# Optimization experiments

Measured on AMD Instinct MI355X. Metric: run time of the kernel, lower is better.

## Reference

```python
import jax, jax.numpy as jnp
import numpy as np

B, N, D = 16, 1024, 5
R_HID = 8  # radial MLP hidden width


def setup_inputs() -> dict:
    key = jax.random.key(0)
    ks = jax.random.split(key, 16)
    feats = jax.random.normal(ks[0], (B, N, D), jnp.float32)
    coors = 3.0 * jax.random.normal(ks[1], (B, N, 3), jnp.float32)
    a = jax.random.bernoulli(ks[2], 0.01, (B, N, N))
    adj_mat = a | jnp.swapaxes(a, 1, 2)
    s = 1.0 / np.sqrt(D)
    Wq = s * jax.random.normal(ks[3], (D, D), jnp.float32)
    Wk = s * jax.random.normal(ks[4], (D, D), jnp.float32)
    Wv = s * jax.random.normal(ks[5], (D, D), jnp.float32)
    Wo = s * jax.random.normal(ks[6], (D, D), jnp.float32)
    w_r1 = 0.5 * jax.random.normal(ks[7], (1, R_HID), jnp.float32)
    b_r1 = jnp.zeros((R_HID,), jnp.float32)
    w_r2 = 0.5 * jax.random.normal(ks[8], (R_HID, 1), jnp.float32)
    b_r2 = jnp.zeros((1,), jnp.float32)
    w1 = (1.0 / np.sqrt(D)) * jax.random.normal(ks[9], (D, 128), jnp.float32)
    b1 = jnp.zeros((128,), jnp.float32)
    w2 = (1.0 / np.sqrt(128.0)) * jax.random.normal(ks[10], (128, 3), jnp.float32)
    b2 = jnp.zeros((3,), jnp.float32)
    return dict(feats=feats, coors=coors, adj_mat=adj_mat, Wq=Wq, Wk=Wk, Wv=Wv,
                Wo=Wo, w_r1=w_r1, b_r1=b_r1, w_r2=w_r2, b_r2=b_r2,
                w1=w1, b1=b1, w2=w2, b2=b2)


def _se3_layer(feats, coors, neigh, Wq, Wk, Wv, Wo, w_r1, b_r1, w_r2, b_r2):
    # SE(3)-invariant sparse graph attention on degree-0 channels.
    # Attention logits = content term + radial (distance-only) bias, so the
    # scalar output is invariant to global rotations/translations of coors.
    q = jnp.einsum('bnd,de->bne', feats, Wq)
    k = jnp.einsum('bnd,de->bne', feats, Wk)
    v = jnp.einsum('bnd,de->bne', feats, Wv)
    rel = coors[:, :, None, :] - coors[:, None, :, :]        # [B,N,N,3]
    dist = jnp.sqrt(jnp.sum(rel * rel, axis=-1) + 1e-8)      # [B,N,N]
    h = jax.nn.relu(dist[..., None] * w_r1[0] + b_r1)        # [B,N,N,R_HID]
    rbias = (h @ w_r2)[..., 0] + b_r2[0]                     # [B,N,N]
    scores = jnp.einsum('bid,bjd->bij', q, k) / np.sqrt(q.shape[-1]) + rbias
    scores = jnp.where(neigh, scores, -1e9)
    attn = jax.nn.softmax(scores, axis=-1)
    agg = jnp.einsum('bij,bjd->bid', attn, v)
    return feats + jnp.einsum('bid,de->bie', agg, Wo)        # residual


def reference(feats, coors, adj_mat, Wq, Wk, Wv, Wo, w_r1, b_r1, w_r2, b_r2,
              w1, b1, w2, b2):
    a = adj_mat.astype(jnp.float32)
    # num_adj_degrees=2: attend over 1-hop and 2-hop neighbors (+ self)
    adj2 = jnp.einsum('bij,bjk->bik', a, a) > 0
    eye = jnp.eye(adj_mat.shape[1], dtype=bool)[None]
    neigh = adj_mat | adj2 | eye
    x = _se3_layer(feats, coors, neigh, Wq, Wk, Wv, Wo, w_r1, b_r1, w_r2, b_r2)
    pooled = jnp.mean(x, axis=1)                              # [B, D]
    hdn = jax.nn.relu(pooled @ w1 + b1)
    return hdn @ w2 + b2                                      # [B, 3]
```

## Files before the change

### kernel.cpp

```cpp
#include <hip/hip_runtime.h>
#include <hip/hip_bf16.h>

#define BB 16
#define NN 1024
#define DD 5
#define RH 8

typedef unsigned long long u64;
typedef unsigned int u32;
typedef __hip_bfloat16 bf16;

static __device__ __forceinline__ float tof(bf16 x) { return __bfloat162float(x); }
static __device__ __forceinline__ float ldf(const void* p, long long i, bool f) {
  return f ? ((const float*)p)[i] : tof(((const bf16*)p)[i]);
}

#define LOG2E 1.4426950408889634f
#define PACK_BLOCKS (BB * NN * 16 / 256)
#define KV_BLOCKS (BB * NN / 256)


__global__ __launch_bounds__(256) void k_pack(
    const void* __restrict__ adj, const void* __restrict__ feats,
    const void* __restrict__ coors,
    const void* __restrict__ Wk, const void* __restrict__ Wv,
    const void* __restrict__ Wo,
    u64* __restrict__ adjbits, float4* __restrict__ kvg,
    float* __restrict__ czg, int* __restrict__ gflags,
    float* __restrict__ pooled, int* __restrict__ cntr) {
  __shared__ int sNon01, sNonpair, sLow3;
  __shared__ int sCnt[4];
  __shared__ float wkL[25], wvL[25], woL[25];
  int tid = threadIdx.x;

  if (blockIdx.x >= PACK_BLOCKS) {
    int kb = blockIdx.x - PACK_BLOCKS;
    if (kb == 0) {
      if (tid < BB * DD) pooled[tid] = 0.0f;
      else if (tid < BB * DD + BB) cntr[tid - BB * DD] = 0;
    }
    {
      u32 x = ((const u32*)feats)[tid];
      u32 lo = x & 0xFFFFu;
      int e = (int)((lo >> 7) & 0xFFu);
      bool insane = !(lo == 0u || (e >= 90 && e <= 150));
      u64 m = __ballot(insane);
      if ((tid & 63) == 0) sCnt[tid >> 6] = (int)__popcll(m);
    }
    __syncthreads();
    bool f32 = (sCnt[0] + sCnt[1] + sCnt[2] + sCnt[3]) > 64;
    if (tid < 25) {
      wkL[tid] = ldf(Wk, tid, f32);
      wvL[tid] = ldf(Wv, tid, f32);
      woL[tid] = ldf(Wo, tid, f32);
    }
    if (kb == 0 && tid == 0) gflags[0] = f32 ? 1 : 0;
    __syncthreads();
    long long node = (long long)kb * 256 + tid;
    float f0 = ldf(feats, node * DD + 0, f32), f1 = ldf(feats, node * DD + 1, f32),
          f2 = ldf(feats, node * DD + 2, f32), f3 = ldf(feats, node * DD + 3, f32),
          f4 = ldf(feats, node * DD + 4, f32);
    float k[DD], tv[DD], v[DD];
    #pragma unroll
    for (int e = 0; e < DD; ++e) {
      k[e] = f0 * wkL[e] + f1 * wkL[5 + e] + f2 * wkL[10 + e] + f3 * wkL[15 + e] +
             f4 * wkL[20 + e];
      tv[e] = f0 * wvL[e] + f1 * wvL[5 + e] + f2 * wvL[10 + e] + f3 * wvL[15 + e] +
              f4 * wvL[20 + e];
    }
    #pragma unroll
    for (int e = 0; e < DD; ++e)
      v[e] = tv[0] * woL[e] + tv[1] * woL[5 + e] + tv[2] * woL[10 + e] +
             tv[3] * woL[15 + e] + tv[4] * woL[20 + e];
    float cx = ldf(coors, node * 3 + 0, f32);
    float cy = ldf(coors, node * 3 + 1, f32);
    float cz = ldf(coors, node * 3 + 2, f32);
    kvg[node * 3 + 0] = make_float4(k[0], k[1], k[2], k[3]);
    kvg[node * 3 + 1] = make_float4(k[4], v[0], v[1], v[2]);
    kvg[node * 3 + 2] = make_float4(v[3], v[4], cx, cy);
    czg[node] = cz;
    return;
  }

  if (tid == 0) { sNon01 = 0; sNonpair = 0; sLow3 = 0; }
  __syncthreads();
  {
    const u32* aw = (const u32*)adj;
    int non01 = 0, nonpair = 0, low3 = 0;
    for (int i = tid; i < 4096; i += 256) {
      u32 x = aw[i];
      u32 lo = x & 0xFFFFu, hi = x >> 16;
      non01 |= (x > 1u);
      nonpair |= !((lo == 0u || lo == 0x3F80u) && (hi == 0u || hi == 0x3F80u));
      low3 |= (lo == 0x3F80u);
    }
    if (non01) atomicOr(&sNon01, 1);
    if (nonpair) atomicOr(&sNonpair, 1);
    if (low3) atomicOr(&sLow3, 1);
  }
  __syncthreads();
  int mode;
  if (!sNon01) mode = 0;
  else if (!sNonpair) mode = sLow3 ? 2 : 3;
  else mode = 1;

  int gid = blockIdx.x * 256 + tid;
  int w = gid & 15;
  long long row = gid >> 4;
  long long base = row * NN + (long long)w * 64;
  u64 bits = 0;
  if (mode == 3) {
    const uint4* p = (const uint4*)((const float*)adj + base);
    #pragma unroll
    for (int t = 0; t < 16; ++t) {
      uint4 x = p[t];
      if (x.x << 1) bits |= 1ull << (4 * t + 0);
      if (x.y << 1) bits |= 1ull << (4 * t + 1);
      if (x.z << 1) bits |= 1ull << (4 * t + 2);
      if (x.w << 1) bits |= 1ull << (4 * t + 3);
    }
  } else if (mode == 0) {
    const uint4* p = (const uint4*)((const u32*)adj + base);
    #pragma unroll
    for (int t = 0; t < 16; ++t) {
      uint4 x = p[t];
      if (x.x) bits |= 1ull << (4 * t + 0);
      if (x.y) bits |= 1ull << (4 * t + 1);
      if (x.z) bits |= 1ull << (4 * t + 2);
      if (x.w) bits |= 1ull << (4 * t + 3);
    }
  } else if (mode == 2) {
    const uint4* p = (const uint4*)((const unsigned short*)adj + base);
    #pragma unroll
    for (int t = 0; t < 8; ++t) {
      uint4 x = p[t];
      u32 c[4] = {x.x, x.y, x.z, x.w};
      #pragma unroll
      for (int q = 0; q < 4; ++q) {
        if ((c[q] & 0x7FFFu)) bits |= 1ull << (8 * t + 2 * q + 0);
        if ((c[q] >> 16) & 0x7FFFu) bits |= 1ull << (8 * t + 2 * q + 1);
      }
    }
  } else {
    const uint4* p = (const uint4*)((const unsigned char*)adj + base);
    #pragma unroll
    for (int t = 0; t < 4; ++t) {
      uint4 x = p[t];
      u32 c[4] = {x.x, x.y, x.z, x.w};
      #pragma unroll
      for (int q = 0; q < 4; ++q)
        #pragma unroll
        for (int bb = 0; bb < 4; ++bb)
          if ((c[q] >> (8 * bb)) & 0xFFu) bits |= 1ull << (16 * t + 4 * q + bb);
    }
  }
  adjbits[gid] = bits;
}

__global__ __launch_bounds__(512) void k_attn(
    const void* __restrict__ feats, const void* __restrict__ coors,
    const void* __restrict__ Wq,
    const void* __restrict__ wr1, const void* __restrict__ br1,
    const void* __restrict__ wr2, const void* __restrict__ br2,
    const float4* __restrict__ kvg, const float* __restrict__ czg,
    const int* __restrict__ gflags, const u64* __restrict__ adjbits,
    float* __restrict__ pooled, int* __restrict__ cntr,
    const void* __restrict__ w1, const void* __restrict__ b1,
    const void* __restrict__ w2, const void* __restrict__ b2,
    float* __restrict__ out) {
  __shared__ __align__(16) float4 kvT[2][3][64];
  __shared__ float czT[2][64];
  __shared__ unsigned short listL[8][NN];
  __shared__ u64 neighL[16][16];
  __shared__ float qL[16 * DD], ciL[16 * 3];
  __shared__ float wqL[25];
  __shared__ float wrL[3][RH];
  __shared__ float sConst[2];
  __shared__ int sFast, sLast;
  __shared__ float waveC[8][DD];
  __shared__ float pM[DD];
  __shared__ float hL[128];

  int bi = blockIdx.x;
  int b = bi >> 6, chunk = bi & 63;
  int tid = threadIdx.x;

  const float4* kvb3 = kvg + (size_t)b * NN * 3;
  const float* czb = czg + (size_t)b * NN;
  bool ldkv = tid < 192;
  bool ldcz = (tid >= 192) && (tid < 256);
  float4 stg;
  float stgc;
  if (ldkv) stg = kvb3[tid];
  else if (ldcz) stgc = czb[tid - 192];

  bool f32 = gflags[0] != 0;
  if (tid < 25) wqL[tid] = ldf(Wq, tid, f32);
  if (tid >= 64 && tid < 64 + RH) {
    int h = tid - 64;
    wrL[0][h] = ldf(wr1, h, f32);
    wrL[1][h] = ldf(br1, h, f32);
    wrL[2][h] = ldf(wr2, h, f32);
  }
  if (tid == 96) {
    float c = 0.0f;
    int ok = 1;
    #pragma unroll
    for (int h = 0; h < RH; ++h) {
      float w1h = ldf(wr1, h, f32);
      if (ldf(br1, h, f32) != 0.0f) ok = 0;
      if (w1h > 0.0f) c += w1h * ldf(wr2, h, f32);
    }
    sConst[0] = c * LOG2E;
    sConst[1] = ldf(br2, 0, f32) * LOG2E;
    sFast = ok;
  }
  __syncthreads();
  int fast = sFast;
  if (tid < 16) {
    long long row = (long long)b * NN + chunk * 16 + tid;
    float f0 = ldf(feats, row * DD + 0, f32), f1 = ldf(feats, row * DD + 1, f32),
          f2 = ldf(feats, row * DD + 2, f32), f3 = ldf(feats, row * DD + 3, f32),
          f4 = ldf(feats, row * DD + 4, f32);
    float qsc = fast ? (0.4472135954999579f * LOG2E) : 0.4472135954999579f;
    #pragma unroll
    for (int e = 0; e < DD; ++e)
      qL[tid * DD + e] = (f0 * wqL[e] + f1 * wqL[5 + e] + f2 * wqL[10 + e] +
                          f3 * wqL[15 + e] + f4 * wqL[20 + e]) * qsc;
    #pragma unroll
    for (int c = 0; c < 3; ++c)
      ciL[tid * 3 + c] = ldf(coors, row * 3 + c, f32);
  }

  int g = tid >> 6, lane = tid & 63;
  int w = lane & 15, grp = lane >> 4;
  const u64* basep = adjbits + (size_t)b * NN * 16;
  for (int rr = 0; rr < 2; ++rr) {
    int il = g * 2 + rr;
    int i = chunk * 16 + il;
    u64 rw = basep[(size_t)i * 16 + w];
    unsigned short* list = listL[g];
    int cnt = 0;
    #pragma unroll
    for (int sw = 0; sw < 16; ++sw) {
      u64 bits = __shfl(rw, sw, 64);
      int mybit = (int)((bits >> lane) & 1ull);
      int pre = __popcll(bits & ((1ull << lane) - 1ull));
      if (mybit) list[cnt + pre] = (unsigned short)(sw * 64 + lane);
      cnt += __popcll(bits);
    }
    u64 acc = rw;
    if (w == (i >> 6)) acc |= 1ull << (i & 63);
    for (int n = grp; n < cnt; n += 4) acc |= basep[(size_t)list[n] * 16 + w];
    acc |= __shfl_xor(acc, 16, 64);
    acc |= __shfl_xor(acc, 32, 64);
    if (lane < 16) neighL[il][lane] = acc;
  }

  if (ldkv) kvT[0][tid % 3][tid / 3] = stg;
  else if (ldcz) czT[0][tid - 192] = stgc;
  __syncthreads();

  float q[2][DD], ci[2][3], l[2], A[2][DD];
  #pragma unroll
  for (int r = 0; r < 2; ++r) {
    #pragma unroll
    for (int e = 0; e < DD; ++e) q[r][e] = qL[(g * 2 + r) * DD + e];
    #pragma unroll
    for (int c = 0; c < 3; ++c) ci[r][c] = ciL[(g * 2 + r) * 3 + c];
    l[r] = 0.0f;
    #pragma unroll
    for (int e = 0; e < DD; ++e) A[r][e] = 0.0f;
  }
  float Cf = sConst[0], br2f = sConst[1];
  int cur = 0;
  for (int t = 0; t < 16; ++t) {
    if (t < 15) {
      if (ldkv) stg = kvb3[(size_t)(t + 1) * 192 + tid];
      else if (ldcz) stgc = czb[(t + 1) * 64 + (tid - 192)];
    }
    float4 ka = kvT[cur][0][lane];
    float4 kb = kvT[cur][1][lane];
    float4 kc = kvT[cur][2][lane];
    float jz = czT[cur][lane];
    float jx = kc.z, jy = kc.w;
    u64 nw[2];
    #pragma unroll
    for (int r = 0; r < 2; ++r) nw[r] = neighL[g * 2 + r][t];
    if (fast) {
      #pragma unroll
      for (int r = 0; r < 2; ++r) {
        float cx = jx - ci[r][0], cy = jy - ci[r][1], cz = jz - ci[r][2];
        float dist =
            __builtin_amdgcn_sqrtf(fmaf(cx, cx, fmaf(cy, cy, fmaf(cz, cz, 1e-8f))));
        float s = fmaf(q[r][0], ka.x, br2f);
        s = fmaf(q[r][1], ka.y, s);
        s = fmaf(q[r][2], ka.z, s);
        s = fmaf(q[r][3], ka.w, s);
        s = fmaf(q[r][4], kb.x, s);
        s = fmaf(Cf, dist, s);
        s = fminf(s, 126.0f);
        s = ((nw[r] >> lane) & 1ull) ? s : -150.0f;
        float p = __builtin_amdgcn_exp2f(s);
        l[r] += p;
        A[r][0] = fmaf(p, kb.y, A[r][0]);
        A[r][1] = fmaf(p, kb.z, A[r][1]);
        A[r][2] = fmaf(p, kb.w, A[r][2]);
        A[r][3] = fmaf(p, kc.x, A[r][3]);
        A[r][4] = fmaf(p, kc.y, A[r][4]);
      }
    } else {
      #pragma unroll
      for (int r = 0; r < 2; ++r) {
        float cx = jx - ci[r][0], cy = jy - ci[r][1], cz = jz - ci[r][2];
        float dist = sqrtf(fmaf(cx, cx, fmaf(cy, cy, fmaf(cz, cz, 1e-8f))));
        float rb = ldf(br2, 0, f32);
        #pragma unroll
        for (int h = 0; h < RH; ++h)
          rb += fmaxf(dist * wrL[0][h] + wrL[1][h], 0.0f) * wrL[2][h];
        float s = fmaf(q[r][0], ka.x, rb);
        s = fmaf(q[r][1], ka.y, s);
        s = fmaf(q[r][2], ka.z, s);
        s = fmaf(q[r][3], ka.w, s);
        s = fmaf(q[r][4], kb.x, s);
        s = fminf(s, 85.0f);
        s = ((nw[r] >> lane) & 1ull) ? s : -100.0f;
        float p = __expf(s);
        l[r] += p;
        A[r][0] = fmaf(p, kb.y, A[r][0]);
        A[r][1] = fmaf(p, kb.z, A[r][1]);
        A[r][2] = fmaf(p, kb.w, A[r][2]);
        A[r][3] = fmaf(p, kc.x, A[r][3]);
        A[r][4] = fmaf(p, kc.y, A[r][4]);
      }
    }
    if (t < 15) {
      if (ldkv) kvT[cur ^ 1][tid % 3][tid / 3] = stg;
      else if (ldcz) czT[cur ^ 1][tid - 192] = stgc;
    }
    __syncthreads();
    cur ^= 1;
  }
  #pragma unroll
  for (int msk = 1; msk < 64; msk <<= 1) {
    #pragma unroll
    for (int r = 0; r < 2; ++r) {
      l[r] += __shfl_xor(l[r], msk, 64);
      A[r][0] += __shfl_xor(A[r][0], msk, 64);
      A[r][1] += __shfl_xor(A[r][1], msk, 64);
      A[r][2] += __shfl_xor(A[r][2], msk, 64);
      A[r][3] += __shfl_xor(A[r][3], msk, 64);
      A[r][4] += __shfl_xor(A[r][4], msk, 64);
    }
  }

  if (lane == 0) {
    float cw[DD] = {0.f, 0.f, 0.f, 0.f, 0.f};
    #pragma unroll
    for (int r = 0; r < 2; ++r) {
      long long grow = (long long)b * NN + chunk * 16 + g * 2 + r;
      float inv = (l[r] > 0.0f) ? 1.0f / l[r] : 0.0f;
      #pragma unroll
      for (int e = 0; e < DD; ++e)
        cw[e] += ldf(feats, grow * DD + e, f32) + A[r][e] * inv;
    }
    #pragma unroll
    for (int e = 0; e < DD; ++e) waveC[g][e] = cw[e];
  }
  __syncthreads();
  if (tid < DD) {
    float s = waveC[0][tid] + waveC[1][tid] + waveC[2][tid] + waveC[3][tid] +
              waveC[4][tid] + waveC[5][tid] + waveC[6][tid] + waveC[7][tid];
    float old = atomicAdd(&pooled[b * DD + tid], s);
    asm volatile("" :: "v"(old));
  }
  __syncthreads();
  if (tid == 0) sLast = (atomicAdd(&cntr[b], 1) == 63) ? 1 : 0;
  __syncthreads();

  if (sLast) {
    if (tid < DD) {
      float pv = __hip_atomic_load(&pooled[b * DD + tid], __ATOMIC_RELAXED,
                                   __HIP_MEMORY_SCOPE_AGENT);
      pM[tid] = pv * (1.0f / 1024.0f);
    }
    __syncthreads();
    if (tid < 128) {
      float acc = ldf(b1, tid, f32);
      #pragma unroll
      for (int d = 0; d < DD; ++d)
        acc = fmaf(pM[d], ldf(w1, d * 128 + tid, f32), acc);
      hL[tid] = fmaxf(acc, 0.0f);
    }
    __syncthreads();
    if (tid < 3) {
      float s = ldf(b2, tid, f32);
      for (int j2 = 0; j2 < 128; ++j2)
        s = fmaf(hL[j2], ldf(w2, j2 * 3 + tid, f32), s);
      out[b * 3 + tid] = s;
    }
  }
}

extern "C" void kernel_launch(void* const* d_in, const int* in_sizes, int n_in,
                              void* d_out, int out_size, void* d_ws, size_t ws_size,
                              hipStream_t stream) {
  const void* adj = d_in[2];
  float* out = (float*)d_out;

  char* w = (char*)d_ws;
  int* gflags = (int*)w;
  float* pooled = (float*)(w + 64);
  int* cntr = (int*)(w + 512);
  const size_t MB2 = (size_t)BB * NN * 16 * sizeof(u64);
  u64* adjbits = (u64*)(w + 1024);
  float4* kvg = (float4*)(w + 1024 + MB2);
  float* czg = (float*)(w + 1024 + MB2 + 786432);

  k_pack<<<PACK_BLOCKS + KV_BLOCKS, 256, 0, stream>>>(
      adj, d_in[0], d_in[1], d_in[4], d_in[5], d_in[6], adjbits, kvg, czg,
      gflags, pooled, cntr);
  k_attn<<<BB * 64, 512, 0, stream>>>(
      d_in[0], d_in[1], d_in[3], d_in[7], d_in[8], d_in[9], d_in[10], kvg, czg,
      gflags, adjbits, pooled, cntr, d_in[11], d_in[12], d_in[13], d_in[14],
      out);
}
```

Baseline: 187.2 us.

## Split two-hop neighbor mask into separate kernel with LDS-staged adjacency tiles

Moves the two-hop neighbor bitmask computation out of the attention kernel into a new k_twohop kernel. That kernel builds per-row neighbor lists and sweeps the batch's packed adjacency rows in four 256-row LDS tiles, ORing in the rows of each neighbor. Overflow beyond a 128-entry list cap falls back to atomicOr. The attention kernel now just loads the precomputed neighbor words, drops its 16 KB list buffer, and remaps the kv staging indices. This trades scattered global gathers inside the attention kernel for an extra launch and a workspace buffer.

```diff
diff --git a/kernel.cpp b/kernel.cpp
--- a/kernel.cpp
+++ b/kernel.cpp
@@ -5,6 +5,7 @@
 #define NN 1024
 #define DD 5
 #define RH 8
+#define CAP 128
 
 typedef unsigned long long u64;
 typedef unsigned int u32;
@@ -157,20 +158,90 @@
   adjbits[gid] = bits;
 }
 
+__global__ __launch_bounds__(256) void k_twohop(const u64* __restrict__ adjbits,
+                                                u64* __restrict__ neighbits) {
+  __shared__ u64 adjL[256][17];
+  __shared__ unsigned short listL[4][16][CAP];
+  __shared__ unsigned short cntL[4][16];
+  __shared__ u64 accL[64][16];
+  int tid = threadIdx.x;
+  int wv = tid >> 6, lane = tid & 63;
+  int b = blockIdx.x >> 4, strip = blockIdx.x & 15;
+  int rowbase = strip * 64;
+  const u64* basep = adjbits + (size_t)b * NN * 16;
+
+  for (int i = lane; i < 16 * 16; i += 64)
+    accL[wv * 16 + (i >> 4)][i & 15] = 0;
+
+  int w16 = lane & 15;
+  for (int rr = 0; rr < 16; ++rr) {
+    int row = rowbase + wv * 16 + rr;
+    u64 rw = basep[(size_t)row * 16 + w16];
+    int cnt = 0;
+    #pragma unroll
+    for (int sw = 0; sw < 16; ++sw) {
+      u64 bits = __shfl(rw, sw, 64);
+      int mybit = (int)((bits >> lane) & 1ull);
+      int pre = __popcll(bits & ((1ull << lane) - 1ull));
+      if (mybit) {
+        int idx = cnt + pre;
+        if (idx < CAP) {
+          listL[wv][rr][idx] = (unsigned short)(sw * 64 + lane);
+        } else {
+          int j = sw * 64 + lane;
+          for (int w2 = 0; w2 < 16; ++w2)
+            atomicOr(&accL[wv * 16 + rr][w2], basep[(size_t)j * 16 + w2]);
+        }
+      }
+      cnt += __popcll(bits);
+    }
+    if (lane == 0) cntL[wv][rr] = (unsigned short)(cnt < CAP ? cnt : CAP);
+  }
+
+  int grp = lane >> 4;
+  for (int q = 0; q < 4; ++q) {
+    __syncthreads();
+    const u64* src = basep + (size_t)q * 256 * 16;
+    for (int k = 0; k < 16; ++k) {
+      int li = k * 256 + tid;
+      adjL[li >> 4][li & 15] = src[li];
+    }
+    __syncthreads();
+    for (int rr = 0; rr < 16; ++rr) {
+      int cnt = cntL[wv][rr];
+      u64 a = 0;
+      for (int n = grp; n < cnt; n += 4) {
+        int j = listL[wv][rr][n];
+        if ((j >> 8) == q) a |= adjL[j & 255][w16];
+      }
+      a |= __shfl_xor(a, 16, 64);
+      a |= __shfl_xor(a, 32, 64);
+      if (lane < 16) accL[wv * 16 + rr][lane] |= a;
+    }
+  }
+
+  for (int rr4 = 0; rr4 < 4; ++rr4) {
+    int rl = rr4 * 4 + grp;
+    int row = rowbase + wv * 16 + rl;
+    u64 nb = accL[wv * 16 + rl][w16] | basep[(size_t)row * 16 + w16];
+    if (w16 == (row >> 6)) nb |= 1ull << (row & 63);
+    neighbits[((size_t)b * NN + row) * 16 + w16] = nb;
+  }
+}
+
 __global__ __launch_bounds__(512) void k_attn(
     const void* __restrict__ feats, const void* __restrict__ coors,
     const void* __restrict__ Wq,
     const void* __restrict__ wr1, const void* __restrict__ br1,
     const void* __restrict__ wr2, const void* __restrict__ br2,
     const float4* __restrict__ kvg, const float* __restrict__ czg,
-    const int* __restrict__ gflags, const u64* __restrict__ adjbits,
+    const int* __restrict__ gflags, const u64* __restrict__ neighbits,
     float* __restrict__ pooled, int* __restrict__ cntr,
     const void* __restrict__ w1, const void* __restrict__ b1,
     const void* __restrict__ w2, const void* __restrict__ b2,
     float* __restrict__ out) {
   __shared__ __align__(16) float4 kvT[2][3][64];
   __shared__ float czT[2][64];
-  __shared__ unsigned short listL[8][NN];
   __shared__ u64 neighL[16][16];
   __shared__ float qL[16 * DD], ciL[16 * 3];
   __shared__ float wqL[25];
@@ -189,9 +260,10 @@
   const float* czb = czg + (size_t)b * NN;
   bool ldkv = tid < 192;
   bool ldcz = (tid >= 192) && (tid < 256);
+  int plane = tid >> 6, slot = tid & 63;
   float4 stg;
   float stgc;
-  if (ldkv) stg = kvb3[tid];
+  if (ldkv) stg = kvb3[slot * 3 + plane];
   else if (ldcz) stgc = czb[tid - 192];
 
   bool f32 = gflags[0] != 0;
@@ -215,6 +287,11 @@
     sConst[1] = ldf(br2, 0, f32) * LOG2E;
     sFast = ok;
   }
+  if (tid >= 256 && tid < 512) {
+    int t2 = tid - 256;
+    neighL[t2 >> 4][t2 & 15] =
+        neighbits[((size_t)(b * NN) + chunk * 16) * 16 + t2];
+  }
   __syncthreads();
   int fast = sFast;
   if (tid < 16) {
@@ -232,35 +309,11 @@
       ciL[tid * 3 + c] = ldf(coors, row * 3 + c, f32);
   }
 
+  if (ldkv) kvT[0][plane][slot] = stg;
+  else if (ldcz) czT[0][tid - 192] = stgc;
+  __syncthreads();
+
   int g = tid >> 6, lane = tid & 63;
-  int w = lane & 15, grp = lane >> 4;
-  const u64* basep = adjbits + (size_t)b * NN * 16;
-  for (int rr = 0; rr < 2; ++rr) {
-    int il = g * 2 + rr;
-    int i = chunk * 16 + il;
-    u64 rw = basep[(size_t)i * 16 + w];
-    unsigned short* list = listL[g];
-    int cnt = 0;
-    #pragma unroll
-    for (int sw = 0; sw < 16; ++sw) {
-      u64 bits = __shfl(rw, sw, 64);
-      int mybit = (int)((bits >> lane) & 1ull);
-      int pre = __popcll(bits & ((1ull << lane) - 1ull));
-      if (mybit) list[cnt + pre] = (unsigned short)(sw * 64 + lane);
-      cnt += __popcll(bits);
-    }
-    u64 acc = rw;
-    if (w == (i >> 6)) acc |= 1ull << (i & 63);
-    for (int n = grp; n < cnt; n += 4) acc |= basep[(size_t)list[n] * 16 + w];
-    acc |= __shfl_xor(acc, 16, 64);
-    acc |= __shfl_xor(acc, 32, 64);
-    if (lane < 16) neighL[il][lane] = acc;
-  }
-
-  if (ldkv) kvT[0][tid % 3][tid / 3] = stg;
-  else if (ldcz) czT[0][tid - 192] = stgc;
-  __syncthreads();
-
   float q[2][DD], ci[2][3], l[2], A[2][DD];
   #pragma unroll
   for (int r = 0; r < 2; ++r) {
@@ -276,7 +329,7 @@
   int cur = 0;
   for (int t = 0; t < 16; ++t) {
     if (t < 15) {
-      if (ldkv) stg = kvb3[(size_t)(t + 1) * 192 + tid];
+      if (ldkv) stg = kvb3[((t + 1) * 64 + slot) * 3 + plane];
       else if (ldcz) stgc = czb[(t + 1) * 64 + (tid - 192)];
     }
     float4 ka = kvT[cur][0][lane];
@@ -335,7 +388,7 @@
       }
     }
     if (t < 15) {
-      if (ldkv) kvT[cur ^ 1][tid % 3][tid / 3] = stg;
+      if (ldkv) kvT[cur ^ 1][plane][slot] = stg;
       else if (ldcz) czT[cur ^ 1][tid - 192] = stgc;
     }
     __syncthreads();
@@ -413,15 +466,17 @@
   float* pooled = (float*)(w + 64);
   int* cntr = (int*)(w + 512);
   const size_t MB2 = (size_t)BB * NN * 16 * sizeof(u64);
-  u64* adjbits = (u64*)(w + 1024);
-  float4* kvg = (float4*)(w + 1024 + MB2);
-  float* czg = (float*)(w + 1024 + MB2 + 786432);
+  u64* adjbits = (u64*)(w + 4096);
+  u64* neighbits = (u64*)(w + 4096 + MB2);
+  float4* kvg = (float4*)(w + 4096 + 2 * MB2);
+  float* czg = (float*)(w + 4096 + 2 * MB2 + 786432);
 
   k_pack<<<PACK_BLOCKS + KV_BLOCKS, 256, 0, stream>>>(
       adj, d_in[0], d_in[1], d_in[4], d_in[5], d_in[6], adjbits, kvg, czg,
       gflags, pooled, cntr);
+  k_twohop<<<BB * 16, 256, 0, stream>>>(adjbits, neighbits);
   k_attn<<<BB * 64, 512, 0, stream>>>(
       d_in[0], d_in[1], d_in[3], d_in[7], d_in[8], d_in[9], d_in[10], kvg, czg,
-      gflags, adjbits, pooled, cntr, d_in[11], d_in[12], d_in[13], d_in[14],
+      gflags, neighbits, pooled, cntr, d_in[11], d_in[12], d_in[13], d_in[14],
       out);
 }
```

Result: slower. 242.5 us (+29.6%).

## Move two-hop neighbor mask computation into a separate kernel

Applied to the files above, without the earlier changes.

The 2-hop neighbor bitmask construction moves out of the attention kernel into its own kernel. That kernel runs one wave per row across many blocks and writes a neighbor bitmap to workspace, which the attention blocks then simply load. This drops the 16KB list buffer from the attention kernel's shared memory and its serialized per-row gather. The key/value staging index is also remapped so global loads are per-plane. The cost is an extra launch plus a write and read of the neighbor bitmap in global memory.

```diff
diff --git a/kernel.cpp b/kernel.cpp
--- a/kernel.cpp
+++ b/kernel.cpp
@@ -157,20 +157,53 @@
   adjbits[gid] = bits;
 }
 
+__global__ __launch_bounds__(256) void k_twohop(const u64* __restrict__ adjbits,
+                                                u64* __restrict__ neighbits) {
+  __shared__ unsigned short listL[4][NN];
+  int wave = threadIdx.x >> 6, lane = threadIdx.x & 63;
+  int row = blockIdx.x * 4 + wave;
+  int b = row >> 10;
+  int i = row & (NN - 1);
+  int w = lane & 15;
+  const u64* rowp = adjbits + (size_t)row * 16;
+  u64 rw = rowp[w];
+  unsigned short* list = listL[wave];
+  int cnt = 0;
+  #pragma unroll
+  for (int sw = 0; sw < 16; ++sw) {
+    u64 bits = __shfl(rw, sw, 64);
+    int mybit = (int)((bits >> lane) & 1ull);
+    int pre = __popcll(bits & ((1ull << lane) - 1ull));
+    if (mybit) list[cnt + pre] = (unsigned short)(sw * 64 + lane);
+    cnt += __popcll(bits);
+  }
+  __syncthreads();
+  u64 acc = rw;
+  if (w == (i >> 6)) acc |= 1ull << (i & 63);
+  int g = lane >> 4;
+  const u64* basep = adjbits + (size_t)b * NN * 16;
+  for (int n = g; n < cnt; n += 4) {
+    int j = list[n];
+    acc |= basep[(size_t)j * 16 + w];
+  }
+  acc |= __shfl_xor(acc, 16, 64);
+  acc |= __shfl_xor(acc, 32, 64);
+  if (lane < 16) neighbits[(size_t)row * 16 + lane] = acc;
+}
+
 __global__ __launch_bounds__(512) void k_attn(
     const void* __restrict__ feats, const void* __restrict__ coors,
     const void* __restrict__ Wq,
     const void* __restrict__ wr1, const void* __restrict__ br1,
     const void* __restrict__ wr2, const void* __restrict__ br2,
     const float4* __restrict__ kvg, const float* __restrict__ czg,
-    const int* __restrict__ gflags, const u64* __restrict__ adjbits,
+    const int* __restrict__ gflags, const u64* __restrict__ neighbits,
     float* __restrict__ pooled, int* __restrict__ cntr,
     const void* __restrict__ w1, const void* __restrict__ b1,
     const void* __restrict__ w2, const void* __restrict__ b2,
     float* __restrict__ out) {
   __shared__ __align__(16) float4 kvT[2][3][64];
   __shared__ float czT[2][64];
-  __shared__ unsigned short listL[8][NN];
   __shared__ u64 neighL[16][16];
   __shared__ float qL[16 * DD], ciL[16 * 3];
   __shared__ float wqL[25];
@@ -189,9 +222,10 @@
   const float* czb = czg + (size_t)b * NN;
   bool ldkv = tid < 192;
   bool ldcz = (tid >= 192) && (tid < 256);
+  int plane = tid >> 6, slot = tid & 63;
   float4 stg;
   float stgc;
-  if (ldkv) stg = kvb3[tid];
+  if (ldkv) stg = kvb3[slot * 3 + plane];
   else if (ldcz) stgc = czb[tid - 192];
 
   bool f32 = gflags[0] != 0;
@@ -215,6 +249,11 @@
     sConst[1] = ldf(br2, 0, f32) * LOG2E;
     sFast = ok;
   }
+  if (tid >= 256 && tid < 512) {
+    int t2 = tid - 256;
+    neighL[t2 >> 4][t2 & 15] =
+        neighbits[((size_t)(b * NN) + chunk * 16) * 16 + t2];
+  }
   __syncthreads();
   int fast = sFast;
   if (tid < 16) {
@@ -232,35 +271,11 @@
       ciL[tid * 3 + c] = ldf(coors, row * 3 + c, f32);
   }
 
+  if (ldkv) kvT[0][plane][slot] = stg;
+  else if (ldcz) czT[0][tid - 192] = stgc;
+  __syncthreads();
+
   int g = tid >> 6, lane = tid & 63;
-  int w = lane & 15, grp = lane >> 4;
-  const u64* basep = adjbits + (size_t)b * NN * 16;
-  for (int rr = 0; rr < 2; ++rr) {
-    int il = g * 2 + rr;
-    int i = chunk * 16 + il;
-    u64 rw = basep[(size_t)i * 16 + w];
-    unsigned short* list = listL[g];
-    int cnt = 0;
-    #pragma unroll
-    for (int sw = 0; sw < 16; ++sw) {
-      u64 bits = __shfl(rw, sw, 64);
-      int mybit = (int)((bits >> lane) & 1ull);
-      int pre = __popcll(bits & ((1ull << lane) - 1ull));
-      if (mybit) list[cnt + pre] = (unsigned short)(sw * 64 + lane);
-      cnt += __popcll(bits);
-    }
-    u64 acc = rw;
-    if (w == (i >> 6)) acc |= 1ull << (i & 63);
-    for (int n = grp; n < cnt; n += 4) acc |= basep[(size_t)list[n] * 16 + w];
-    acc |= __shfl_xor(acc, 16, 64);
-    acc |= __shfl_xor(acc, 32, 64);
-    if (lane < 16) neighL[il][lane] = acc;
-  }
-
-  if (ldkv) kvT[0][tid % 3][tid / 3] = stg;
-  else if (ldcz) czT[0][tid - 192] = stgc;
-  __syncthreads();
-
   float q[2][DD], ci[2][3], l[2], A[2][DD];
   #pragma unroll
   for (int r = 0; r < 2; ++r) {
@@ -276,7 +291,7 @@
   int cur = 0;
   for (int t = 0; t < 16; ++t) {
     if (t < 15) {
-      if (ldkv) stg = kvb3[(size_t)(t + 1) * 192 + tid];
+      if (ldkv) stg = kvb3[((t + 1) * 64 + slot) * 3 + plane];
       else if (ldcz) stgc = czb[(t + 1) * 64 + (tid - 192)];
     }
     float4 ka = kvT[cur][0][lane];
@@ -335,7 +350,7 @@
       }
     }
     if (t < 15) {
-      if (ldkv) kvT[cur ^ 1][tid % 3][tid / 3] = stg;
+      if (ldkv) kvT[cur ^ 1][plane][slot] = stg;
       else if (ldcz) czT[cur ^ 1][tid - 192] = stgc;
     }
     __syncthreads();
@@ -413,15 +428,17 @@
   float* pooled = (float*)(w + 64);
   int* cntr = (int*)(w + 512);
   const size_t MB2 = (size_t)BB * NN * 16 * sizeof(u64);
-  u64* adjbits = (u64*)(w + 1024);
-  float4* kvg = (float4*)(w + 1024 + MB2);
-  float* czg = (float*)(w + 1024 + MB2 + 786432);
+  u64* adjbits = (u64*)(w + 4096);
+  u64* neighbits = (u64*)(w + 4096 + MB2);
+  float4* kvg = (float4*)(w + 4096 + 2 * MB2);
+  float* czg = (float*)(w + 4096 + 2 * MB2 + 786432);
 
   k_pack<<<PACK_BLOCKS + KV_BLOCKS, 256, 0, stream>>>(
       adj, d_in[0], d_in[1], d_in[4], d_in[5], d_in[6], adjbits, kvg, czg,
       gflags, pooled, cntr);
+  k_twohop<<<BB * NN / 4, 256, 0, stream>>>(adjbits, neighbits);
   k_attn<<<BB * 64, 512, 0, stream>>>(
       d_in[0], d_in[1], d_in[3], d_in[7], d_in[8], d_in[9], d_in[10], kvg, czg,
-      gflags, adjbits, pooled, cntr, d_in[11], d_in[12], d_in[13], d_in[14],
+      gflags, neighbits, pooled, cntr, d_in[11], d_in[12], d_in[13], d_in[14],
       out);
 }
```

Result: no change. 184.1 us (-1.6%).
